# Optimization experiments

Measured on AMD Instinct MI355X. Metric: run time of the kernel, lower is better.

## Reference

```python
import jax, jax.numpy as jnp
import numpy as np

N_NODES = 100000
N_EDGES = 600000
HIDDEN = 128
BN_EPS = 1e-5


def setup_inputs() -> dict:
    key = jax.random.key(0)
    k_x, k_e, k_w, k_b, k_g = jax.random.split(key, 5)
    x = jax.random.normal(k_x, (N_NODES, HIDDEN), dtype=jnp.float32)
    edge_index = jax.random.randint(k_e, (2, N_EDGES), 0, N_NODES, dtype=jnp.int64)
    # GCNConv linear weight (no bias on the linear; bias added post-aggregation)
    scale = 1.0 / np.sqrt(HIDDEN)
    W = jax.random.uniform(k_w, (HIDDEN, HIDDEN), jnp.float32, -scale, scale)
    b = jax.random.uniform(k_b, (HIDDEN,), jnp.float32, -scale, scale)
    gamma = jnp.ones((HIDDEN,), jnp.float32)   # BatchNorm weight
    beta = jnp.zeros((HIDDEN,), jnp.float32)   # BatchNorm bias
    return {"x": x, "edge_index": edge_index, "W": W, "b": b, "gamma": gamma, "beta": beta}


def reference(x, edge_index, W, b, gamma, beta):
    N = x.shape[0]
    # ReLU then GCNConv linear transform: [N, D]
    h = jnp.matmul(jax.nn.relu(x), W)
    # Add self-loops (PyG GCNConv default)
    loops = jnp.arange(N, dtype=edge_index.dtype)
    row = jnp.concatenate([edge_index[0], loops])  # source nodes
    col = jnp.concatenate([edge_index[1], loops])  # target nodes
    # Symmetric normalization deg^{-1/2} with unit edge weights
    ones = jnp.ones(row.shape[0], dtype=h.dtype)
    deg = jax.ops.segment_sum(ones, col, num_segments=N)
    dinv = jnp.where(deg > 0, jax.lax.rsqrt(deg), 0.0)
    norm = dinv[row] * dinv[col]  # [E+N]
    # Gather -> scale -> scatter-add aggregation, then conv bias
    agg = jax.ops.segment_sum(norm[:, None] * h[row], col, num_segments=N)
    out = agg + b
    # BatchNorm1d (training mode: batch stats, biased variance)
    mean = jnp.mean(out, axis=0)
    var = jnp.var(out, axis=0)
    return gamma * (out - mean) * jax.lax.rsqrt(var + BN_EPS) + beta
```

## Files before the change

kernel.cpp:

```cpp
#include <hip/hip_runtime.h>

#define D 128
#define CAP 40
#define BN_EPS 1e-5f

typedef float floatx4 __attribute__((ext_vector_type(4)));
typedef __bf16 bf16x8 __attribute__((ext_vector_type(8)));

__device__ inline unsigned short f2bf(float f) {
    unsigned u; __builtin_memcpy(&u, &f, 4);
    unsigned r = (u + 0x7FFFu + ((u >> 16) & 1u)) >> 16;
    return (unsigned short)r;
}
__device__ inline float bflo(unsigned v) { unsigned x = v << 16; float f; __builtin_memcpy(&f, &x, 4); return f; }
__device__ inline float bfhi(unsigned v) { unsigned x = v & 0xFFFF0000u; float f; __builtin_memcpy(&f, &x, 4); return f; }

__global__ void setup_k(const unsigned* __restrict__ e, int* __restrict__ flag,
                        int* __restrict__ cursor, float* __restrict__ sums,
                        float* __restrict__ sumsq, int n_nodes) {
    int i = blockIdx.x * blockDim.x + threadIdx.x;
    if (i < n_nodes) cursor[i] = 0;
    if (i < D) { sums[i] = 0.f; sumsq[i] = 0.f; }
    if (i == 0) {
        unsigned acc = 0;
        for (int k = 0; k < 64; ++k) acc |= e[2 * k + 1];
        *flag = (acc == 0u) ? 1 : 0;
    }
}

__global__ __launch_bounds__(256, 2) void gemm_k(const float* __restrict__ x,
                                                 const float* __restrict__ W,
                                                 unsigned short* __restrict__ h,
                                                 int n_mtiles) {
    int lane = threadIdx.x & 63;
    int wave = blockIdx.x * 4 + (threadIdx.x >> 6);
    int nw = gridDim.x * 4;
    int l15 = lane & 15;
    int quad = lane >> 4;

    bf16x8 Bf[4][8];
    for (int ks = 0; ks < 4; ++ks)
        for (int j = 0; j < 8; ++j) {
            union { unsigned short u[8]; bf16x8 v; } tmp;
            int n = j * 16 + l15;
            for (int jj = 0; jj < 8; ++jj) {
                int k = ks * 32 + quad * 8 + jj;
                tmp.u[jj] = f2bf(W[k * D + n]);
            }
            Bf[ks][j] = tmp.v;
        }

    for (int mt = wave; mt < n_mtiles; mt += nw) {
        const float* xrow = x + (size_t)(mt * 16 + l15) * D + quad * 8;
        bf16x8 Af[4];
        for (int ks = 0; ks < 4; ++ks) {
            float4 a0 = *(const float4*)(xrow + ks * 32);
            float4 a1 = *(const float4*)(xrow + ks * 32 + 4);
            float av[8] = {a0.x, a0.y, a0.z, a0.w, a1.x, a1.y, a1.z, a1.w};
            union { unsigned short u[8]; bf16x8 v; } tmp;
            for (int jj = 0; jj < 8; ++jj) tmp.u[jj] = f2bf(fmaxf(av[jj], 0.0f));
            Af[ks] = tmp.v;
        }
        floatx4 acc[8];
        for (int j = 0; j < 8; ++j) acc[j] = (floatx4){0.f, 0.f, 0.f, 0.f};
        for (int ks = 0; ks < 4; ++ks)
            for (int j = 0; j < 8; ++j)
                acc[j] = __builtin_amdgcn_mfma_f32_16x16x32_bf16(Af[ks], Bf[ks][j], acc[j], 0, 0, 0);
        for (int j = 0; j < 8; ++j)
            for (int reg = 0; reg < 4; ++reg) {
                int rr = mt * 16 + quad * 4 + reg;
                int cc = j * 16 + l15;
                h[(size_t)rr * D + cc] = f2bf(acc[j][reg]);
            }
    }
}

__global__ __launch_bounds__(256) void bucket_k(const void* __restrict__ ep, const int* __restrict__ flag,
                                                int* __restrict__ cursor, int* __restrict__ bucket,
                                                int n_edges) {
    int e = blockIdx.x * blockDim.x + threadIdx.x;
    if (e >= n_edges) return;
    int r, c;
    if (*flag) {
        const long long* p = (const long long*)ep;
        r = (int)p[e]; c = (int)p[e + n_edges];
    } else {
        const int* p = (const int*)ep;
        r = p[e]; c = p[e + n_edges];
    }
    int pos = atomicAdd(&cursor[c], 1);
    if (pos < CAP) bucket[(size_t)c * CAP + pos] = r;
}

__global__ void dinv_k(const int* __restrict__ cursor, float* __restrict__ dinv, int n_nodes) {
    int i = blockIdx.x * blockDim.x + threadIdx.x;
    if (i < n_nodes) dinv[i] = rsqrtf(1.0f + (float)cursor[i]);
}

__global__ __launch_bounds__(256) void agg_k(const unsigned short* __restrict__ h,
                                             const int* __restrict__ bucket, const int* __restrict__ cursor,
                                             const float* __restrict__ dinv,
                                             unsigned* __restrict__ aggb,
                                             float* __restrict__ sums, float* __restrict__ sumsq,
                                             int n_nodes) {
    __shared__ float red[256];
    int lane = threadIdx.x & 63;
    int wib = threadIdx.x >> 6;
    int wave = blockIdx.x * 4 + wib;
    int nw = gridDim.x * 4;
    const unsigned* hp = (const unsigned*)h;

    float s0 = 0.f, s1 = 0.f, q0 = 0.f, q1 = 0.f;

    for (int node = wave; node < n_nodes; node += nw) {
        float dc = dinv[node];
        unsigned v = hp[(size_t)node * 64 + lane];
        float ax = dc * bflo(v), ay = dc * bfhi(v);
        int deg = cursor[node]; if (deg > CAP) deg = CAP;
        const int* bk = bucket + (size_t)node * CAP;
        int e = 0;
        for (; e + 4 <= deg; e += 4) {
            int4 r4 = *(const int4*)(bk + e);
            float d0 = dinv[r4.x], d1 = dinv[r4.y], d2 = dinv[r4.z], d3 = dinv[r4.w];
            unsigned h0 = hp[(size_t)r4.x * 64 + lane];
            unsigned h1 = hp[(size_t)r4.y * 64 + lane];
            unsigned h2 = hp[(size_t)r4.z * 64 + lane];
            unsigned h3 = hp[(size_t)r4.w * 64 + lane];
            ax += d0 * bflo(h0); ay += d0 * bfhi(h0);
            ax += d1 * bflo(h1); ay += d1 * bfhi(h1);
            ax += d2 * bflo(h2); ay += d2 * bfhi(h2);
            ax += d3 * bflo(h3); ay += d3 * bfhi(h3);
        }
        for (; e < deg; ++e) {
            int r = bk[e];
            float dr = dinv[r];
            unsigned hv = hp[(size_t)r * 64 + lane];
            ax += dr * bflo(hv); ay += dr * bfhi(hv);
        }
        float ox = dc * ax, oy = dc * ay;
        s0 += ox; s1 += oy; q0 += ox * ox; q1 += oy * oy;
        aggb[(size_t)node * 64 + lane] = ((unsigned)f2bf(oy) << 16) | (unsigned)f2bf(ox);
    }

    red[threadIdx.x] = s0; __syncthreads();
    if (wib == 0) atomicAdd(&sums[2 * lane], red[lane] + red[64 + lane] + red[128 + lane] + red[192 + lane]);
    __syncthreads();
    red[threadIdx.x] = s1; __syncthreads();
    if (wib == 0) atomicAdd(&sums[2 * lane + 1], red[lane] + red[64 + lane] + red[128 + lane] + red[192 + lane]);
    __syncthreads();
    red[threadIdx.x] = q0; __syncthreads();
    if (wib == 0) atomicAdd(&sumsq[2 * lane], red[lane] + red[64 + lane] + red[128 + lane] + red[192 + lane]);
    __syncthreads();
    red[threadIdx.x] = q1; __syncthreads();
    if (wib == 0) atomicAdd(&sumsq[2 * lane + 1], red[lane] + red[64 + lane] + red[128 + lane] + red[192 + lane]);
}

__global__ void params_k(const float* __restrict__ sums, const float* __restrict__ sumsq,
                         const float* __restrict__ gamma, const float* __restrict__ beta,
                         float* __restrict__ scale, float* __restrict__ shift, int n_nodes) {
    int f = threadIdx.x;
    float inv_n = 1.0f / (float)n_nodes;
    float mean = sums[f] * inv_n;
    float var = sumsq[f] * inv_n - mean * mean;
    float sc = gamma[f] * rsqrtf(var + BN_EPS);
    scale[f] = sc;
    shift[f] = beta[f] - mean * sc;
}

__global__ __launch_bounds__(256) void final_k(const unsigned* __restrict__ aggb,
                                               const float* __restrict__ scale, const float* __restrict__ shift,
                                               float* __restrict__ out, int total4) {
    int i = blockIdx.x * blockDim.x + threadIdx.x;
    if (i >= total4) return;
    int idx = i * 4;
    int f = idx & (D - 1);
    uint2 p = *(const uint2*)(aggb + i * 2);
    float4 sc = *(const float4*)(scale + f);
    float4 sh = *(const float4*)(shift + f);
    float4 o;
    o.x = fmaf(bflo(p.x), sc.x, sh.x);
    o.y = fmaf(bfhi(p.x), sc.y, sh.y);
    o.z = fmaf(bflo(p.y), sc.z, sh.z);
    o.w = fmaf(bfhi(p.y), sc.w, sh.w);
    *(float4*)(out + idx) = o;
}

extern "C" void kernel_launch(void* const* d_in, const int* in_sizes, int n_in,
                              void* d_out, int out_size, void* d_ws, size_t ws_size,
                              hipStream_t stream) {
    const float* x     = (const float*)d_in[0];
    const void*  edges = d_in[1];
    const float* W     = (const float*)d_in[2];
    const float* gamma = (const float*)d_in[4];
    const float* beta  = (const float*)d_in[5];
    float* out = (float*)d_out;

    int N = in_sizes[0] / D;
    int E = in_sizes[1] / 2;

    char* ws = (char*)d_ws;
    size_t off = 0;
    auto alloc = [&](size_t bytes) { void* p = ws + off; off += (bytes + 255) & ~(size_t)255; return p; };
    unsigned short* h = (unsigned short*)alloc((size_t)N * D * 2);
    unsigned* aggb    = (unsigned*)alloc((size_t)N * D * 2);
    int* bucket       = (int*)alloc((size_t)N * CAP * 4);
    int* cursor       = (int*)alloc((size_t)N * 4);
    float* dinv       = (float*)alloc((size_t)N * 4);
    float* sums       = (float*)alloc(512);
    float* sumsq      = (float*)alloc(512);
    float* scale      = (float*)alloc(512);
    float* shift      = (float*)alloc(512);
    int* flag         = (int*)alloc(16);

    int nblk = (N + 255) / 256;
    int n_mtiles = N / 16;

    setup_k<<<nblk, 256, 0, stream>>>((const unsigned*)edges, flag, cursor, sums, sumsq, N);
    gemm_k<<<256, 256, 0, stream>>>(x, W, h, n_mtiles);
    bucket_k<<<(E + 255) / 256, 256, 0, stream>>>(edges, flag, cursor, bucket, E);
    dinv_k<<<nblk, 256, 0, stream>>>(cursor, dinv, N);
    agg_k<<<1024, 256, 0, stream>>>(h, bucket, cursor, dinv, aggb, sums, sumsq, N);
    params_k<<<1, 128, 0, stream>>>(sums, sumsq, gamma, beta, scale, shift, N);
    final_k<<<(N * D / 4 + 255) / 256, 256, 0, stream>>>(aggb, scale, shift, out, N * D / 4);
}
```

Before: 266.7 us.

## Pre-transpose W to bf16, inline dinv, unroll aggregation, split stats, fold BN params

W is transposed and converted to bf16 once in the setup kernel, so each GEMM wave loads its B fragments as vectors instead of doing strided scalar converts; the GEMM grid is enlarged. The dinv and params kernels are removed: degree normalisation is computed inline from cursor, and the BN scale/shift is recomputed per element in final_k. Aggregation now uses one node per wave with up to 16 neighbour loads issued before accumulation, to expose more memory-level parallelism. BN statistics move to a separate kernel that rereads aggb, which costs an extra pass over that buffer and adds redundant rsqrt work.

```diff
diff --git a/kernel.cpp b/kernel.cpp
--- a/kernel.cpp
+++ b/kernel.cpp
@@ -17,10 +17,15 @@
 
 __global__ void setup_k(const unsigned* __restrict__ e, int* __restrict__ flag,
                         int* __restrict__ cursor, float* __restrict__ sums,
-                        float* __restrict__ sumsq, int n_nodes) {
+                        float* __restrict__ sumsq, const float* __restrict__ W,
+                        unsigned short* __restrict__ Wt, int n_nodes) {
     int i = blockIdx.x * blockDim.x + threadIdx.x;
     if (i < n_nodes) cursor[i] = 0;
     if (i < D) { sums[i] = 0.f; sumsq[i] = 0.f; }
+    if (i < D * D) {
+        int n = i >> 7, k = i & 127;
+        Wt[n * D + k] = f2bf(W[k * D + n]);
+    }
     if (i == 0) {
         unsigned acc = 0;
         for (int k = 0; k < 64; ++k) acc |= e[2 * k + 1];
@@ -29,7 +34,7 @@
 }
 
 __global__ __launch_bounds__(256, 2) void gemm_k(const float* __restrict__ x,
-                                                 const float* __restrict__ W,
+                                                 const unsigned short* __restrict__ Wt,
                                                  unsigned short* __restrict__ h,
                                                  int n_mtiles) {
     int lane = threadIdx.x & 63;
@@ -40,15 +45,8 @@
 
     bf16x8 Bf[4][8];
     for (int ks = 0; ks < 4; ++ks)
-        for (int j = 0; j < 8; ++j) {
-            union { unsigned short u[8]; bf16x8 v; } tmp;
-            int n = j * 16 + l15;
-            for (int jj = 0; jj < 8; ++jj) {
-                int k = ks * 32 + quad * 8 + jj;
-                tmp.u[jj] = f2bf(W[k * D + n]);
-            }
-            Bf[ks][j] = tmp.v;
-        }
+        for (int j = 0; j < 8; ++j)
+            Bf[ks][j] = *(const bf16x8*)(Wt + (size_t)(j * 16 + l15) * D + ks * 32 + quad * 8);
 
     for (int mt = wave; mt < n_mtiles; mt += nw) {
         const float* xrow = x + (size_t)(mt * 16 + l15) * D + quad * 8;
@@ -92,56 +90,65 @@
     if (pos < CAP) bucket[(size_t)c * CAP + pos] = r;
 }
 
-__global__ void dinv_k(const int* __restrict__ cursor, float* __restrict__ dinv, int n_nodes) {
-    int i = blockIdx.x * blockDim.x + threadIdx.x;
-    if (i < n_nodes) dinv[i] = rsqrtf(1.0f + (float)cursor[i]);
-}
+#define PREP(s, rr) { int r_ = ((s) < degc) ? (rr) : node;                              \
+                      w##s = ((s) < degc) ? rsqrtf(1.0f + (float)cursor[r_]) : 0.0f;    \
+                      hv##s = hp[(size_t)r_ * 64 + lane]; }
+#define ACC(s) { ax += w##s * bflo(hv##s); ay += w##s * bfhi(hv##s); }
 
 __global__ __launch_bounds__(256) void agg_k(const unsigned short* __restrict__ h,
-                                             const int* __restrict__ bucket, const int* __restrict__ cursor,
-                                             const float* __restrict__ dinv,
+                                             const int* __restrict__ bucket,
+                                             const int* __restrict__ cursor,
                                              unsigned* __restrict__ aggb,
-                                             float* __restrict__ sums, float* __restrict__ sumsq,
                                              int n_nodes) {
+    int lane = threadIdx.x & 63;
+    int node = blockIdx.x * 4 + (threadIdx.x >> 6);
+    if (node >= n_nodes) return;
+    const unsigned* hp = (const unsigned*)h;
+
+    int deg = cursor[node];
+    float dc = rsqrtf(1.0f + (float)deg);
+    int degc = deg < CAP ? deg : CAP;
+
+    unsigned v = hp[(size_t)node * 64 + lane];
+    float ax = dc * bflo(v), ay = dc * bfhi(v);
+    const int* bk = bucket + (size_t)node * CAP;
+
+    float w0=0,w1=0,w2=0,w3=0,w4=0,w5=0,w6=0,w7=0,w8=0,w9=0,w10=0,w11=0,w12=0,w13=0,w14=0,w15=0;
+    unsigned hv0=0,hv1=0,hv2=0,hv3=0,hv4=0,hv5=0,hv6=0,hv7=0,hv8=0,hv9=0,hv10=0,hv11=0,hv12=0,hv13=0,hv14=0,hv15=0;
+
+    if (degc > 0)  { int4 b = *(const int4*)(bk);      PREP(0,b.x)  PREP(1,b.y)  PREP(2,b.z)  PREP(3,b.w)  }
+    if (degc > 4)  { int4 b = *(const int4*)(bk + 4);  PREP(4,b.x)  PREP(5,b.y)  PREP(6,b.z)  PREP(7,b.w)  }
+    if (degc > 8)  { int4 b = *(const int4*)(bk + 8);  PREP(8,b.x)  PREP(9,b.y)  PREP(10,b.z) PREP(11,b.w) }
+    if (degc > 12) { int4 b = *(const int4*)(bk + 12); PREP(12,b.x) PREP(13,b.y) PREP(14,b.z) PREP(15,b.w) }
+
+    ACC(0)  ACC(1)  ACC(2)  ACC(3)  ACC(4)  ACC(5)  ACC(6)  ACC(7)
+    ACC(8)  ACC(9)  ACC(10) ACC(11) ACC(12) ACC(13) ACC(14) ACC(15)
+
+    for (int e = 16; e < degc; ++e) {
+        int r = bk[e];
+        float dr = rsqrtf(1.0f + (float)cursor[r]);
+        unsigned hh = hp[(size_t)r * 64 + lane];
+        ax += dr * bflo(hh); ay += dr * bfhi(hh);
+    }
+
+    float ox = dc * ax, oy = dc * ay;
+    aggb[(size_t)node * 64 + lane] = ((unsigned)f2bf(oy) << 16) | (unsigned)f2bf(ox);
+}
+
+__global__ __launch_bounds__(256) void stats_k(const unsigned* __restrict__ aggb,
+                                               float* __restrict__ sums, float* __restrict__ sumsq,
+                                               int n_nodes) {
     __shared__ float red[256];
     int lane = threadIdx.x & 63;
     int wib = threadIdx.x >> 6;
     int wave = blockIdx.x * 4 + wib;
     int nw = gridDim.x * 4;
-    const unsigned* hp = (const unsigned*)h;
-
     float s0 = 0.f, s1 = 0.f, q0 = 0.f, q1 = 0.f;
-
-    for (int node = wave; node < n_nodes; node += nw) {
-        float dc = dinv[node];
-        unsigned v = hp[(size_t)node * 64 + lane];
-        float ax = dc * bflo(v), ay = dc * bfhi(v);
-        int deg = cursor[node]; if (deg > CAP) deg = CAP;
-        const int* bk = bucket + (size_t)node * CAP;
-        int e = 0;
-        for (; e + 4 <= deg; e += 4) {
-            int4 r4 = *(const int4*)(bk + e);
-            float d0 = dinv[r4.x], d1 = dinv[r4.y], d2 = dinv[r4.z], d3 = dinv[r4.w];
-            unsigned h0 = hp[(size_t)r4.x * 64 + lane];
-            unsigned h1 = hp[(size_t)r4.y * 64 + lane];
-            unsigned h2 = hp[(size_t)r4.z * 64 + lane];
-            unsigned h3 = hp[(size_t)r4.w * 64 + lane];
-            ax += d0 * bflo(h0); ay += d0 * bfhi(h0);
-            ax += d1 * bflo(h1); ay += d1 * bfhi(h1);
-            ax += d2 * bflo(h2); ay += d2 * bfhi(h2);
-            ax += d3 * bflo(h3); ay += d3 * bfhi(h3);
-        }
-        for (; e < deg; ++e) {
-            int r = bk[e];
-            float dr = dinv[r];
-            unsigned hv = hp[(size_t)r * 64 + lane];
-            ax += dr * bflo(hv); ay += dr * bfhi(hv);
-        }
-        float ox = dc * ax, oy = dc * ay;
-        s0 += ox; s1 += oy; q0 += ox * ox; q1 += oy * oy;
-        aggb[(size_t)node * 64 + lane] = ((unsigned)f2bf(oy) << 16) | (unsigned)f2bf(ox);
-    }
-
+    for (int n = wave; n < n_nodes; n += nw) {
+        unsigned p = aggb[(size_t)n * 64 + lane];
+        float vx = bflo(p), vy = bfhi(p);
+        s0 += vx; s1 += vy; q0 += vx * vx; q1 += vy * vy;
+    }
     red[threadIdx.x] = s0; __syncthreads();
     if (wib == 0) atomicAdd(&sums[2 * lane], red[lane] + red[64 + lane] + red[128 + lane] + red[192 + lane]);
     __syncthreads();
@@ -155,33 +162,30 @@
     if (wib == 0) atomicAdd(&sumsq[2 * lane + 1], red[lane] + red[64 + lane] + red[128 + lane] + red[192 + lane]);
 }
 
-__global__ void params_k(const float* __restrict__ sums, const float* __restrict__ sumsq,
-                         const float* __restrict__ gamma, const float* __restrict__ beta,
-                         float* __restrict__ scale, float* __restrict__ shift, int n_nodes) {
-    int f = threadIdx.x;
-    float inv_n = 1.0f / (float)n_nodes;
-    float mean = sums[f] * inv_n;
-    float var = sumsq[f] * inv_n - mean * mean;
-    float sc = gamma[f] * rsqrtf(var + BN_EPS);
-    scale[f] = sc;
-    shift[f] = beta[f] - mean * sc;
-}
-
 __global__ __launch_bounds__(256) void final_k(const unsigned* __restrict__ aggb,
-                                               const float* __restrict__ scale, const float* __restrict__ shift,
-                                               float* __restrict__ out, int total4) {
+                                               const float* __restrict__ sums, const float* __restrict__ sumsq,
+                                               const float* __restrict__ gamma, const float* __restrict__ beta,
+                                               float* __restrict__ out, int total4, float inv_n) {
     int i = blockIdx.x * blockDim.x + threadIdx.x;
     if (i >= total4) return;
     int idx = i * 4;
     int f = idx & (D - 1);
+    float4 sm = *(const float4*)(sums + f);
+    float4 sq = *(const float4*)(sumsq + f);
+    float4 g  = *(const float4*)(gamma + f);
+    float4 bt = *(const float4*)(beta + f);
     uint2 p = *(const uint2*)(aggb + i * 2);
-    float4 sc = *(const float4*)(scale + f);
-    float4 sh = *(const float4*)(shift + f);
+
+    float m0 = sm.x * inv_n, m1 = sm.y * inv_n, m2 = sm.z * inv_n, m3 = sm.w * inv_n;
+    float sc0 = g.x * rsqrtf(sq.x * inv_n - m0 * m0 + BN_EPS);
+    float sc1 = g.y * rsqrtf(sq.y * inv_n - m1 * m1 + BN_EPS);
+    float sc2 = g.z * rsqrtf(sq.z * inv_n - m2 * m2 + BN_EPS);
+    float sc3 = g.w * rsqrtf(sq.w * inv_n - m3 * m3 + BN_EPS);
     float4 o;
-    o.x = fmaf(bflo(p.x), sc.x, sh.x);
-    o.y = fmaf(bfhi(p.x), sc.y, sh.y);
-    o.z = fmaf(bflo(p.y), sc.z, sh.z);
-    o.w = fmaf(bfhi(p.y), sc.w, sh.w);
+    o.x = fmaf(bflo(p.x), sc0, bt.x - m0 * sc0);
+    o.y = fmaf(bfhi(p.x), sc1, bt.y - m1 * sc1);
+    o.z = fmaf(bflo(p.y), sc2, bt.z - m2 * sc2);
+    o.w = fmaf(bfhi(p.y), sc3, bt.w - m3 * sc3);
     *(float4*)(out + idx) = o;
 }
 
@@ -201,25 +205,22 @@
     char* ws = (char*)d_ws;
     size_t off = 0;
     auto alloc = [&](size_t bytes) { void* p = ws + off; off += (bytes + 255) & ~(size_t)255; return p; };
-    unsigned short* h = (unsigned short*)alloc((size_t)N * D * 2);
-    unsigned* aggb    = (unsigned*)alloc((size_t)N * D * 2);
-    int* bucket       = (int*)alloc((size_t)N * CAP * 4);
-    int* cursor       = (int*)alloc((size_t)N * 4);
-    float* dinv       = (float*)alloc((size_t)N * 4);
-    float* sums       = (float*)alloc(512);
-    float* sumsq      = (float*)alloc(512);
-    float* scale      = (float*)alloc(512);
-    float* shift      = (float*)alloc(512);
-    int* flag         = (int*)alloc(16);
+    unsigned short* h  = (unsigned short*)alloc((size_t)N * D * 2);
+    unsigned* aggb     = (unsigned*)alloc((size_t)N * D * 2);
+    int* bucket        = (int*)alloc((size_t)N * CAP * 4);
+    int* cursor        = (int*)alloc((size_t)N * 4);
+    unsigned short* Wt = (unsigned short*)alloc((size_t)D * D * 2);
+    float* sums        = (float*)alloc(512);
+    float* sumsq       = (float*)alloc(512);
+    int* flag          = (int*)alloc(16);
 
     int nblk = (N + 255) / 256;
     int n_mtiles = N / 16;
 
-    setup_k<<<nblk, 256, 0, stream>>>((const unsigned*)edges, flag, cursor, sums, sumsq, N);
-    gemm_k<<<256, 256, 0, stream>>>(x, W, h, n_mtiles);
+    setup_k<<<nblk, 256, 0, stream>>>((const unsigned*)edges, flag, cursor, sums, sumsq, W, Wt, N);
+    gemm_k<<<782, 256, 0, stream>>>(x, Wt, h, n_mtiles);
     bucket_k<<<(E + 255) / 256, 256, 0, stream>>>(edges, flag, cursor, bucket, E);
-    dinv_k<<<nblk, 256, 0, stream>>>(cursor, dinv, N);
-    agg_k<<<1024, 256, 0, stream>>>(h, bucket, cursor, dinv, aggb, sums, sumsq, N);
-    params_k<<<1, 128, 0, stream>>>(sums, sumsq, gamma, beta, scale, shift, N);
-    final_k<<<(N * D / 4 + 255) / 256, 256, 0, stream>>>(aggb, scale, shift, out, N * D / 4);
-}
+    agg_k<<<(N + 3) / 4, 256, 0, stream>>>(h, bucket, cursor, aggb, N);
+    stats_k<<<256, 256, 0, stream>>>(aggb, sums, sumsq, N);
+    final_k<<<(N * D / 4 + 255) / 256, 256, 0, stream>>>(aggb, sums, sumsq, gamma, beta, out, N * D / 4, 1.0f / (float)N);
+}
```

New measurement: 270.5 us. No clear change (+1.4%).
